# Performance work log

Hardware: AMD Instinct MI355X
Metric: run time of the kernel (lower is better)

The kernel has to match this reference:

```python
import jax, jax.numpy as jnp
import numpy as np

FINE_VOCAB = 1_000_000
COARSE_VOCAB = 10_000
D = 128          # embedding_dim
H = 32           # gate hidden width
B, L = 2048, 200 # batch, history length


def setup_inputs() -> dict:
    key = jax.random.key(0)
    ks = jax.random.split(key, 8)
    fine_ids = jax.random.randint(ks[0], (B, L), 0, FINE_VOCAB, dtype=jnp.int64)
    coarse_ids = jax.random.randint(ks[1], (B, L), 0, COARSE_VOCAB, dtype=jnp.int64)
    # embedding tables (xavier-ish scale); padding row 0 zeroed (padding_idx=0)
    fine_W = (jax.random.normal(ks[2], (FINE_VOCAB + 1, D), jnp.float32) * 0.02).at[0].set(0.0)
    coarse_W = (jax.random.normal(ks[3], (COARSE_VOCAB + 1, D), jnp.float32) * 0.02).at[0].set(0.0)
    # freq table initialized to ones, padding row zeroed
    freq_W = jnp.ones((FINE_VOCAB + 1, 1), jnp.float32).at[0].set(0.0)
    # gate MLP: Linear(2D+1 -> 32), ReLU, Linear(32 -> 1), Sigmoid
    W1 = jax.random.normal(ks[4], (2 * D + 1, H), jnp.float32) * (1.0 / np.sqrt(2 * D + 1))
    b1 = jnp.zeros((H,), jnp.float32)
    W2 = jax.random.normal(ks[5], (H, 1), jnp.float32) * (1.0 / np.sqrt(H))
    b2 = jnp.zeros((1,), jnp.float32)
    return {"fine_ids": fine_ids, "coarse_ids": coarse_ids, "fine_W": fine_W,
            "coarse_W": coarse_W, "freq_W": freq_W, "W1": W1, "b1": b1,
            "W2": W2, "b2": b2}


def reference(fine_ids, coarse_ids, fine_W, coarse_W, freq_W, W1, b1, W2, b2):
    fine_emb = fine_W[fine_ids]          # [B, L, D]
    coarse_emb = coarse_W[coarse_ids]    # [B, L, D]
    freq_weight = jax.nn.sigmoid(freq_W[fine_ids])  # [B, L, 1]
    combined = jnp.concatenate([fine_emb, coarse_emb, freq_weight], axis=-1)  # [B, L, 2D+1]
    h = jax.nn.relu(combined @ W1 + b1)                 # [B, L, H]
    gate = jax.nn.sigmoid(h @ W2 + b2)                  # [B, L, 1]
    adjusted_gate = gate * freq_weight                  # [B, L, 1]
    fused = adjusted_gate * fine_emb + (1.0 - adjusted_gate) * coarse_emb
    return fused, adjusted_gate
```

## Files before the change

kernel.cpp:

```cpp
#include <hip/hip_runtime.h>
#include <math.h>


#define DD 128
#define HH 32

typedef float  f32x4  __attribute__((ext_vector_type(4)));
typedef short  bf16x8 __attribute__((ext_vector_type(8)));

__device__ __forceinline__ float sigmoid_f(float x) {
    return 1.0f / (1.0f + expf(-x));
}

__device__ __forceinline__ unsigned short bf16_rne(float x) {
    union { float f; unsigned u; } c; c.f = x;
    unsigned u = c.u + 0x7fffu + ((c.u >> 16) & 1u);
    return (unsigned short)(u >> 16);
}

__global__ __launch_bounds__(256) void coarse_mlp_kernel(
    const float* __restrict__ coarse_W,
    const float* __restrict__ W1,
    const float* __restrict__ b1,
    float* __restrict__ hc,
    int nCoarse)
{
    const int t = blockIdx.x * 256 + threadIdx.x;
    if (t >= nCoarse * HH) return;
    const int r = t >> 5;
    const int j = t & 31;
    const float* __restrict__ row = coarse_W + (size_t)r * DD;
    const float* __restrict__ w   = W1 + DD * HH + j;
    float acc = b1[j];
    #pragma unroll 8
    for (int i = 0; i < DD; ++i)
        acc = fmaf(row[i], w[i * HH], acc);
    hc[t] = acc;
}

__global__ __launch_bounds__(256, 5) void fused_kernel(
    const int*   __restrict__ fine_ids,
    const int*   __restrict__ coarse_ids,
    const float* __restrict__ fine_W,
    const float* __restrict__ coarse_W,
    const float* __restrict__ freq_W,
    const float* __restrict__ W1,
    const float* __restrict__ W2,
    const float* __restrict__ b2,
    const float* __restrict__ hc,
    float* __restrict__ out_fused,
    float* __restrict__ out_gate)
{
    __shared__ __align__(16) unsigned int sX[4][1024];
    __shared__ __align__(16) unsigned int sW1f[2048];
    __shared__ float s_fw[256];
    __shared__ int   s_if[256];
    __shared__ int   s_ic[256];

    const int tid  = threadIdx.x;
    const int lane = tid & 63;
    const int wave = tid >> 6;
    const int P0   = (int)blockIdx.x * 256;

    const int jlo  = lane & 15;
    const int kg   = lane >> 4;
    const int l32  = lane & 31;
    const int hsel = lane >> 5;

    {
        const int p = P0 + tid;
        const int idf = fine_ids[p];
        s_if[tid] = idf;
        s_ic[tid] = coarse_ids[p];
        s_fw[tid] = sigmoid_f(freq_W[idf]);
    }

    #pragma unroll
    for (int n = 0; n < 2; ++n)
        #pragma unroll
        for (int ks = 0; ks < 4; ++ks) {
            bf16x8 t;
            #pragma unroll
            for (int i = 0; i < 8; ++i) {
                const int k = ks * 32 + kg * 8 + i;
                t[i] = (short)bf16_rne(W1[k * HH + jlo + 16 * n]);
            }
            *(bf16x8*)((char*)sW1f + (n * 4 + ks) * 1024 + lane * 16) = t;
        }

    const float w256_0 = W1[2 * DD * HH + jlo];
    const float w256_1 = W1[2 * DD * HH + jlo + 16];
    const float W2_0   = W2[jlo];
    const float W2_1   = W2[jlo + 16];
    const float b2v    = b2[0];

    __syncthreads();

    char* const swave = (char*)&sX[wave][0];
    const int wbase = wave * 64;

    #pragma unroll 1
    for (int it = 0; it < 4; ++it) {
        const int base = wbase + it * 16;

        unsigned pkA[8], pkB[8];
        #pragma unroll
        for (int i = 0; i < 8; ++i) {
            const int idf = s_if[base + 2 * i + hsel];
            const float4 v = *(const float4*)(fine_W + (size_t)idf * DD + 4 * l32);
            pkA[i] = (unsigned)bf16_rne(v.x) | ((unsigned)bf16_rne(v.y) << 16);
            pkB[i] = (unsigned)bf16_rne(v.z) | ((unsigned)bf16_rne(v.w) << 16);
        }

        #pragma unroll
        for (int i = 0; i < 8; ++i) {
            const int row = 2 * i + hsel;
            uint2 w2; w2.x = pkA[i]; w2.y = pkB[i];
            *(uint2*)(swave + row * 256 + ((8 * l32) ^ ((row & 7) << 4))) = w2;
        }

        float hc0[4], hc1[4];
        #pragma unroll
        for (int r = 0; r < 4; ++r) {
            const int idc = s_ic[base + kg * 4 + r];
            const float* __restrict__ hcrow = hc + idc * HH;
            hc0[r] = hcrow[jlo];
            hc1[r] = hcrow[jlo + 16];
        }

        f32x4 acc0 = {0.f, 0.f, 0.f, 0.f};
        f32x4 acc1 = {0.f, 0.f, 0.f, 0.f};
        #pragma unroll
        for (int ks = 0; ks < 4; ++ks) {
            const bf16x8 a = *(const bf16x8*)(swave
                + jlo * 256 + ((kg * 16 + ks * 64) ^ ((jlo & 7) << 4)));
            const bf16x8 b0 = *(const bf16x8*)((char*)sW1f + ks * 1024 + lane * 16);
            const bf16x8 b1 = *(const bf16x8*)((char*)sW1f + (4 + ks) * 1024 + lane * 16);
            acc0 = __builtin_amdgcn_mfma_f32_16x16x32_bf16(a, b0, acc0, 0, 0, 0);
            acc1 = __builtin_amdgcn_mfma_f32_16x16x32_bf16(a, b1, acc1, 0, 0, 0);
        }

        float adjv[4];
        #pragma unroll
        for (int r = 0; r < 4; ++r) {
            const int posl = base + kg * 4 + r;
            const float fw = s_fw[posl];
            const float v0 = acc0[r] + hc0[r] + w256_0 * fw;
            const float v1 = acc1[r] + hc1[r] + w256_1 * fw;
            float tr = fmaxf(v0, 0.f) * W2_0 + fmaxf(v1, 0.f) * W2_1;
            tr += __shfl_xor(tr, 1);
            tr += __shfl_xor(tr, 2);
            tr += __shfl_xor(tr, 4);
            tr += __shfl_xor(tr, 8);
            adjv[r] = sigmoid_f(tr + b2v) * fw;
            if (jlo == r)
                __builtin_nontemporal_store(adjv[r], out_gate + P0 + posl);
        }

        #pragma unroll
        for (int i = 0; i < 8; ++i) {
            const int m0 = 2 * i, m1 = 2 * i + 1;
            const float a0 = __shfl(adjv[m0 & 3], (m0 >> 2) << 4);
            const float a1 = __shfl(adjv[m1 & 3], (m1 >> 2) << 4);
            const float a  = hsel ? a1 : a0;
            const int rowl = 2 * i + hsel;
            const int row  = base + rowl;
            const int idc  = s_ic[row];
            const float4 c4 = *(const float4*)(coarse_W + (size_t)idc * DD + 4 * l32);
            const uint2 w2 = *(const uint2*)(swave
                + rowl * 256 + ((8 * l32) ^ ((rowl & 7) << 4)));
            const float fx = __uint_as_float(w2.x << 16);
            const float fy = __uint_as_float(w2.x & 0xffff0000u);
            const float fz = __uint_as_float(w2.y << 16);
            const float fw4 = __uint_as_float(w2.y & 0xffff0000u);
            f32x4 o;
            o.x = fmaf(a, fx  - c4.x, c4.x);
            o.y = fmaf(a, fy  - c4.y, c4.y);
            o.z = fmaf(a, fz  - c4.z, c4.z);
            o.w = fmaf(a, fw4 - c4.w, c4.w);
            f32x4* dst = (f32x4*)(out_fused + (size_t)(P0 + row) * DD + 4 * l32);
            __builtin_nontemporal_store(o, dst);
        }
    }
}

extern "C" void kernel_launch(void* const* d_in, const int* in_sizes, int n_in,
                              void* d_out, int out_size, void* d_ws, size_t ws_size,
                              hipStream_t stream) {
    const int*   fine_ids   = (const int*)  d_in[0];
    const int*   coarse_ids = (const int*)  d_in[1];
    const float* fine_W     = (const float*)d_in[2];
    const float* coarse_W   = (const float*)d_in[3];
    const float* freq_W     = (const float*)d_in[4];
    const float* W1         = (const float*)d_in[5];
    const float* b1         = (const float*)d_in[6];
    const float* W2         = (const float*)d_in[7];
    const float* b2         = (const float*)d_in[8];

    const int n       = in_sizes[0];
    const int nCoarse = in_sizes[3] / DD;

    float* out_fused = (float*)d_out;
    float* out_gate  = (float*)d_out + (size_t)n * DD;
    float* hc        = (float*)d_ws;

    coarse_mlp_kernel<<<dim3((nCoarse * HH + 255) / 256), dim3(256), 0, stream>>>(
        coarse_W, W1, b1, hc, nCoarse);

    fused_kernel<<<dim3(n / 256), dim3(256), 0, stream>>>(
        fine_ids, coarse_ids, fine_W, coarse_W, freq_W,
        W1, W2, b2, hc, out_fused, out_gate);
}
```

Before: 123.4 us.

## Prefetch next iteration's fine embedding rows into registers and reuse packed values

Loads the fine embedding rows for the next 16-row chunk into registers while the current chunk's MFMA and gate work runs, so gather latency overlaps with compute. It also reuses the packed bf16 register values for the final blend instead of re-reading them from LDS. The launch-bounds occupancy hint drops from 5 to 4 to give the extra live registers room, which costs some latency hiding from wave-level parallelism.

```diff
diff --git a/kernel.cpp b/kernel.cpp
--- a/kernel.cpp
+++ b/kernel.cpp
@@ -38,7 +38,7 @@
     hc[t] = acc;
 }
 
-__global__ __launch_bounds__(256, 5) void fused_kernel(
+__global__ __launch_bounds__(256, 4) void fused_kernel(
     const int*   __restrict__ fine_ids,
     const int*   __restrict__ coarse_ids,
     const float* __restrict__ fine_W,
@@ -99,6 +99,13 @@
     char* const swave = (char*)&sX[wave][0];
     const int wbase = wave * 64;
 
+    float4 fv[8];
+    #pragma unroll
+    for (int i = 0; i < 8; ++i) {
+        const int idf = s_if[wbase + 2 * i + hsel];
+        fv[i] = *(const float4*)(fine_W + (size_t)idf * DD + 4 * l32);
+    }
+
     #pragma unroll 1
     for (int it = 0; it < 4; ++it) {
         const int base = wbase + it * 16;
@@ -106,10 +113,8 @@
         unsigned pkA[8], pkB[8];
         #pragma unroll
         for (int i = 0; i < 8; ++i) {
-            const int idf = s_if[base + 2 * i + hsel];
-            const float4 v = *(const float4*)(fine_W + (size_t)idf * DD + 4 * l32);
-            pkA[i] = (unsigned)bf16_rne(v.x) | ((unsigned)bf16_rne(v.y) << 16);
-            pkB[i] = (unsigned)bf16_rne(v.z) | ((unsigned)bf16_rne(v.w) << 16);
+            pkA[i] = (unsigned)bf16_rne(fv[i].x) | ((unsigned)bf16_rne(fv[i].y) << 16);
+            pkB[i] = (unsigned)bf16_rne(fv[i].z) | ((unsigned)bf16_rne(fv[i].w) << 16);
         }
 
         #pragma unroll
@@ -117,6 +122,14 @@
             const int row = 2 * i + hsel;
             uint2 w2; w2.x = pkA[i]; w2.y = pkB[i];
             *(uint2*)(swave + row * 256 + ((8 * l32) ^ ((row & 7) << 4))) = w2;
+        }
+
+        if (it < 3) {
+            #pragma unroll
+            for (int i = 0; i < 8; ++i) {
+                const int idf = s_if[base + 16 + 2 * i + hsel];
+                fv[i] = *(const float4*)(fine_W + (size_t)idf * DD + 4 * l32);
+            }
         }
 
         float hc0[4], hc1[4];
@@ -163,16 +176,13 @@
             const float a0 = __shfl(adjv[m0 & 3], (m0 >> 2) << 4);
             const float a1 = __shfl(adjv[m1 & 3], (m1 >> 2) << 4);
             const float a  = hsel ? a1 : a0;
-            const int rowl = 2 * i + hsel;
-            const int row  = base + rowl;
+            const int row  = base + 2 * i + hsel;
             const int idc  = s_ic[row];
             const float4 c4 = *(const float4*)(coarse_W + (size_t)idc * DD + 4 * l32);
-            const uint2 w2 = *(const uint2*)(swave
-                + rowl * 256 + ((8 * l32) ^ ((rowl & 7) << 4)));
-            const float fx = __uint_as_float(w2.x << 16);
-            const float fy = __uint_as_float(w2.x & 0xffff0000u);
-            const float fz = __uint_as_float(w2.y << 16);
-            const float fw4 = __uint_as_float(w2.y & 0xffff0000u);
+            const float fx = __uint_as_float(pkA[i] << 16);
+            const float fy = __uint_as_float(pkA[i] & 0xffff0000u);
+            const float fz = __uint_as_float(pkB[i] << 16);
+            const float fw4 = __uint_as_float(pkB[i] & 0xffff0000u);
             f32x4 o;
             o.x = fmaf(a, fx  - c4.x, c4.x);
             o.y = fmaf(a, fy  - c4.y, c4.y);
```

After: 156.2 us. 26.6% more time.
